# Performance work log

Measured on AMD Instinct MI355X. Metric: run time of the kernel, lower is better.

Reference implementation:

```python
import jax, jax.numpy as jnp
import numpy as np

N_RAYS = 65536
S_UNIFORM = 256          # 2 * n_samples coarse samples per ray
N_IMP = 128              # importance samples per ray
TRUNCATION = 2.0 / 512.0 * 4.0  # default in sdf2weights


def raw2weights_occupancy(raw):
    # raw2outputs_nerf_color with occupancy=True
    alpha = jax.nn.sigmoid(10.0 * raw)  # [N, S]
    trans = jnp.cumprod(
        jnp.concatenate([jnp.ones_like(alpha[:, :1]), 1.0 - alpha + 1e-10], axis=-1),
        axis=-1,
    )[:, :-1]
    return alpha, alpha * trans


def sample_pdf_det(bins, weights, n_samples):
    # bins: [N, M], weights: [N, M-1]; deterministic (det=True) inverse-CDF sampling
    w = weights + 1e-5
    pdf = w / jnp.sum(w, axis=-1, keepdims=True)
    cdf = jnp.cumsum(pdf, axis=-1)
    cdf = jnp.concatenate([jnp.zeros_like(cdf[..., :1]), cdf], axis=-1)  # [N, M]
    u = jnp.linspace(0.0, 1.0, n_samples, dtype=cdf.dtype)
    u = jnp.broadcast_to(u, cdf.shape[:-1] + (n_samples,))               # [N, n]
    inds = jax.vmap(lambda c, uu: jnp.searchsorted(c, uu, side='right'))(cdf, u)
    below = jnp.maximum(inds - 1, 0)
    above = jnp.minimum(inds, cdf.shape[-1] - 1)
    cdf_b = jnp.take_along_axis(cdf, below, axis=-1)
    cdf_a = jnp.take_along_axis(cdf, above, axis=-1)
    bins_b = jnp.take_along_axis(bins, below, axis=-1)
    bins_a = jnp.take_along_axis(bins, above, axis=-1)
    denom = cdf_a - cdf_b
    denom = jnp.where(denom < 1e-5, jnp.ones_like(denom), denom)
    t = (u - cdf_b) / denom
    return bins_b + t * (bins_a - bins_b)


def sdf2weights(sdf, z_vals, truncation=TRUNCATION, sc_factor=1.0):
    alpha = jax.nn.sigmoid(sdf / truncation) * jax.nn.sigmoid(-sdf / truncation)
    signs = sdf[:, 1:] * sdf[:, :-1]
    sign_mask = jnp.where(signs < 0.0, 1.0, 0.0)
    inds = jnp.argmax(sign_mask, axis=1)[:, None]              # first zero-crossing
    z_min = jnp.take_along_axis(z_vals, inds, axis=1)          # [N, 1]
    trunc_mask = jnp.where(z_vals < z_min + sc_factor * truncation, 1.0, 0.0)
    alpha = alpha * trunc_mask
    weights = alpha / (jnp.sum(alpha, axis=-1, keepdims=True) + 1e-8)
    return weights


def setup_inputs() -> dict:
    key = jax.random.key(0)
    k1, k2, k3, k4 = jax.random.split(key, 4)
    occ = jax.random.normal(k1, (N_RAYS, S_UNIFORM), dtype=jnp.float32)
    # monotonically increasing depths in [0.1, 4.1)
    z_vals_u = jnp.sort(
        jax.random.uniform(k2, (N_RAYS, S_UNIFORM), dtype=jnp.float32) * 4.0 + 0.1,
        axis=-1,
    )
    sdf = jax.random.normal(k3, (N_RAYS, N_IMP), dtype=jnp.float32) * 0.05
    rgbs = jax.random.uniform(k4, (N_RAYS, N_IMP, 3), dtype=jnp.float32)
    return {"occ": occ, "z_vals_u": z_vals_u, "sdf": sdf, "rgbs": rgbs}


def reference(occ, z_vals_u, sdf, rgbs):
    # 1) coarse occupancy compositing -> weights
    _, w_u = raw2weights_occupancy(occ)
    # 2) inverse-CDF importance sampling over midpoints (detached, as in gen_samples)
    z_mid = 0.5 * (z_vals_u[..., 1:] + z_vals_u[..., :-1])
    z_samples = jax.lax.stop_gradient(sample_pdf_det(z_mid, w_u[..., 1:-1], N_IMP))
    # 3) TSDF weights at importance samples
    weights = sdf2weights(sdf, z_samples)
    # 4) composite
    rgb_map = jnp.clip(jnp.sum(weights[..., None] * rgbs, axis=-2), 0.0, 1.0)  # [N,3]
    depth_map = jnp.sum(weights * z_samples, axis=-1)                          # [N]
    return jnp.concatenate([rgb_map, depth_map[:, None], weights], axis=-1)    # [N, 4+N_IMP]
```

## Files before the change

### kernel.cpp

```cpp
#include <hip/hip_runtime.h>

#define S_U 256
#define N_IMP 128
#define OUT_STRIDE (4 + N_IMP)
#define TRUNC 0.015625f
#define WPB 4

__device__ __forceinline__ float inv_cdf_sample(const float* __restrict__ cdf,
                                                const float* __restrict__ zm,
                                                float u) {
    int lo = 0, hi = 255;
#pragma unroll
    for (int it = 0; it < 8; ++it) {
        int mid = (lo + hi) >> 1;
        bool c = cdf[mid] <= u;
        lo = c ? mid + 1 : lo;
        hi = c ? hi : mid;
    }
    int below = max(lo - 1, 0);
    int above = min(lo, 254);
    float cb = cdf[below], ca = cdf[above];
    float zb = zm[below],  za = zm[above];
    float denom = ca - cb;
    denom = (denom < 1e-5f) ? 1.0f : denom;
    float t = (u - cb) / denom;
    return zb + t * (za - zb);
}

__global__ __launch_bounds__(256) void tsdf_render_kernel(
    const float* __restrict__ occ,
    const float* __restrict__ zvals,
    const float* __restrict__ sdf,
    const float* __restrict__ rgbs,
    float* __restrict__ out)
{
    const int lane = threadIdx.x & 63;
    const int wv   = threadIdx.x >> 6;
    const int ray  = blockIdx.x * WPB + wv;

    __shared__ __align__(16) float s_cdf [WPB][S_U];
    __shared__ __align__(16) float s_zmid[WPB][S_U];

    const float4 o4 = ((const float4*)(occ   + (size_t)ray * S_U))[lane];
    const float4 z4 = ((const float4*)(zvals + (size_t)ray * S_U))[lane];

    float a0 = 1.0f / (1.0f + __expf(-10.0f * o4.x));
    float a1 = 1.0f / (1.0f + __expf(-10.0f * o4.y));
    float a2 = 1.0f / (1.0f + __expf(-10.0f * o4.z));
    float a3 = 1.0f / (1.0f + __expf(-10.0f * o4.w));
    float t0 = 1.0f - a0 + 1e-10f;
    float t1 = 1.0f - a1 + 1e-10f;
    float t2 = 1.0f - a2 + 1e-10f;
    float t3 = 1.0f - a3 + 1e-10f;

    float pp0 = t0, pp1 = pp0 * t1, pp2 = pp1 * t2, pp3 = pp2 * t3;
    float ip = pp3;
#pragma unroll
    for (int d = 1; d < 64; d <<= 1) {
        float y = __shfl_up(ip, d);
        if (lane >= d) ip *= y;
    }
    float pbase = __shfl_up(ip, 1);
    if (lane == 0) pbase = 1.0f;

    float w0 = a0 * pbase;
    float w1 = a1 * pbase * pp0;
    float w2 = a2 * pbase * pp1;
    float w3 = a3 * pbase * pp2;

    float v0 = (lane > 0)  ? w0 + 1e-5f : 0.0f;
    float v1 = w1 + 1e-5f;
    float v2 = w2 + 1e-5f;
    float v3 = (lane < 63) ? w3 + 1e-5f : 0.0f;
    float s0 = v0, s1 = s0 + v1, s2 = s1 + v2, s3 = s2 + v3;
    float is = s3;
#pragma unroll
    for (int d = 1; d < 64; d <<= 1) {
        float y = __shfl_up(is, d);
        if (lane >= d) is += y;
    }
    float total = __shfl(is, 63);
    float sbase = __shfl_up(is, 1);
    if (lane == 0) sbase = 0.0f;
    float invt = 1.0f / total;

    float4 cdf4;
    cdf4.x = (sbase + s0) * invt;
    cdf4.y = (sbase + s1) * invt;
    cdf4.z = (sbase + s2) * invt;
    cdf4.w = (sbase + s3) * invt;
    *((float4*)&s_cdf[wv][lane * 4]) = cdf4;

    float znext = __shfl_down(z4.x, 1);
    float4 zm4;
    zm4.x = 0.5f * (z4.x + z4.y);
    zm4.y = 0.5f * (z4.y + z4.z);
    zm4.z = 0.5f * (z4.z + z4.w);
    zm4.w = 0.5f * (z4.w + znext);
    *((float4*)&s_zmid[wv][lane * 4]) = zm4;

    __builtin_amdgcn_wave_barrier();

    const float2 sd2 = ((const float2*)(sdf + (size_t)ray * N_IMP))[lane];
    const float2* rg = (const float2*)(rgbs + (size_t)ray * (N_IMP * 3)) + lane * 3;
    float2 p0 = rg[0];
    float2 p1 = rg[1];
    float2 p2 = rg[2];

    const float* cdfp = s_cdf[wv];
    const float* zmp  = s_zmid[wv];
    float u0 = (float)(2 * lane)     * (1.0f / 127.0f);
    float u1 = (float)(2 * lane + 1) * (1.0f / 127.0f);
    float zs0 = inv_cdf_sample(cdfp, zmp, u0);
    float zs1 = inv_cdf_sample(cdfp, zmp, u1);

    float sn = __shfl_down(sd2.x, 1);
    int c = 0x7fffffff;
    if (sd2.x * sd2.y < 0.0f)                     c = 2 * lane;
    else if (lane < 63 && sd2.y * sn < 0.0f)      c = 2 * lane + 1;
#pragma unroll
    for (int d = 32; d > 0; d >>= 1) c = min(c, __shfl_xor(c, d));
    int ci = (c == 0x7fffffff) ? 0 : c;
    float zca = __shfl(zs0, ci >> 1);
    float zcb = __shfl(zs1, ci >> 1);
    float z_min = (ci & 1) ? zcb : zca;

    float x0 = sd2.x * (1.0f / TRUNC);
    float x1 = sd2.y * (1.0f / TRUNC);
    float al0 = 1.0f / (2.0f + __expf(x0) + __expf(-x0));
    float al1 = 1.0f / (2.0f + __expf(x1) + __expf(-x1));
    float zlim = z_min + TRUNC;
    if (!(zs0 < zlim)) al0 = 0.0f;
    if (!(zs1 < zlim)) al1 = 0.0f;

    float asum = al0 + al1;
#pragma unroll
    for (int d = 32; d > 0; d >>= 1) asum += __shfl_xor(asum, d);
    float inv_s = 1.0f / (asum + 1e-8f);
    float g0 = al0 * inv_s;
    float g1 = al1 * inv_s;

    float rr = g0 * p0.x + g1 * p1.y;
    float gg = g0 * p0.y + g1 * p2.x;
    float bb = g0 * p1.x + g1 * p2.y;
    float dd = g0 * zs0  + g1 * zs1;
#pragma unroll
    for (int d = 32; d > 0; d >>= 1) {
        rr += __shfl_xor(rr, d);
        gg += __shfl_xor(gg, d);
        bb += __shfl_xor(bb, d);
        dd += __shfl_xor(dd, d);
    }

    float* ob = out + (size_t)ray * OUT_STRIDE;
    ((float2*)(ob + 4))[lane] = make_float2(g0, g1);
    if (lane == 0) {
        ob[0] = fminf(fmaxf(rr, 0.0f), 1.0f);
        ob[1] = fminf(fmaxf(gg, 0.0f), 1.0f);
        ob[2] = fminf(fmaxf(bb, 0.0f), 1.0f);
        ob[3] = dd;
    }
}

extern "C" void kernel_launch(void* const* d_in, const int* in_sizes, int n_in,
                              void* d_out, int out_size, void* d_ws, size_t ws_size,
                              hipStream_t stream) {
    const float* occ  = (const float*)d_in[0];
    const float* z    = (const float*)d_in[1];
    const float* sdf  = (const float*)d_in[2];
    const float* rgbs = (const float*)d_in[3];
    float* out = (float*)d_out;
    const int n_rays = in_sizes[0] / S_U;
    hipLaunchKernelGGL(tsdf_render_kernel, dim3(n_rays / WPB), dim3(256), 0, stream,
                       occ, z, sdf, rgbs, out);
}
```

Baseline: 266.2 us.

## Replace per-sample binary search with scatter-scan bin lookup and DPP wave scans

Swaps the 8-step binary search over the CDF for each importance sample for an inverted approach. Each CDF entry computes which uniform sample index it covers and scatters its bin index into shared memory, and a wave max-scan then gives each sample its bin. All shuffle-based scans and reductions become DPP row and broadcast operations, and all sdf and rgb global loads are moved to the kernel start. Divisions become hardware reciprocal approximations, which may change rounding slightly. The kernel is probably bound by memory bandwidth, so the lower ALU and LDS work may only partly show in the runtime.

```diff
diff --git a/kernel.cpp b/kernel.cpp
--- a/kernel.cpp
+++ b/kernel.cpp
@@ -1,30 +1,69 @@
 #include <hip/hip_runtime.h>
+#include <limits.h>
 
 #define S_U 256
 #define N_IMP 128
 #define OUT_STRIDE (4 + N_IMP)
 #define TRUNC 0.015625f
 #define WPB 4
-
-__device__ __forceinline__ float inv_cdf_sample(const float* __restrict__ cdf,
-                                                const float* __restrict__ zm,
-                                                float u) {
-    int lo = 0, hi = 255;
-#pragma unroll
-    for (int it = 0; it < 8; ++it) {
-        int mid = (lo + hi) >> 1;
-        bool c = cdf[mid] <= u;
-        lo = c ? mid + 1 : lo;
-        hi = c ? hi : mid;
-    }
-    int below = max(lo - 1, 0);
-    int above = min(lo, 254);
-    float cb = cdf[below], ca = cdf[above];
-    float zb = zm[below],  za = zm[above];
-    float denom = ca - cb;
-    denom = (denom < 1e-5f) ? 1.0f : denom;
-    float t = (u - cb) / denom;
-    return zb + t * (za - zb);
+#define INV127 (1.0f / 127.0f)
+
+template<int CTRL, int RM, int BM>
+__device__ __forceinline__ int dpp_i(int old_, int x) {
+    return __builtin_amdgcn_update_dpp(old_, x, CTRL, RM, BM, false);
+}
+template<int CTRL, int RM, int BM>
+__device__ __forceinline__ float dpp_f(float old_, float x) {
+    return __int_as_float(__builtin_amdgcn_update_dpp(
+        __float_as_int(old_), __float_as_int(x), CTRL, RM, BM, false));
+}
+__device__ __forceinline__ float readlane_f(float x, int l) {
+    return __int_as_float(__builtin_amdgcn_readlane(__float_as_int(x), l));
+}
+
+__device__ __forceinline__ float wscan_add(float x) {
+    x += dpp_f<0x111,0xf,0xf>(0.0f, x);
+    x += dpp_f<0x112,0xf,0xf>(0.0f, x);
+    x += dpp_f<0x114,0xf,0xf>(0.0f, x);
+    x += dpp_f<0x118,0xf,0xf>(0.0f, x);
+    x += dpp_f<0x142,0xa,0xf>(0.0f, x);
+    x += dpp_f<0x143,0xc,0xf>(0.0f, x);
+    return x;
+}
+__device__ __forceinline__ float wscan_mul(float x) {
+    x *= dpp_f<0x111,0xf,0xf>(1.0f, x);
+    x *= dpp_f<0x112,0xf,0xf>(1.0f, x);
+    x *= dpp_f<0x114,0xf,0xf>(1.0f, x);
+    x *= dpp_f<0x118,0xf,0xf>(1.0f, x);
+    x *= dpp_f<0x142,0xa,0xf>(1.0f, x);
+    x *= dpp_f<0x143,0xc,0xf>(1.0f, x);
+    return x;
+}
+__device__ __forceinline__ int wscan_max(int x) {
+    x = max(x, dpp_i<0x111,0xf,0xf>(0, x));
+    x = max(x, dpp_i<0x112,0xf,0xf>(0, x));
+    x = max(x, dpp_i<0x114,0xf,0xf>(0, x));
+    x = max(x, dpp_i<0x118,0xf,0xf>(0, x));
+    x = max(x, dpp_i<0x142,0xa,0xf>(0, x));
+    x = max(x, dpp_i<0x143,0xc,0xf>(0, x));
+    return x;
+}
+__device__ __forceinline__ int wred_min(int x) {
+    x = min(x, dpp_i<0x111,0xf,0xf>(INT_MAX, x));
+    x = min(x, dpp_i<0x112,0xf,0xf>(INT_MAX, x));
+    x = min(x, dpp_i<0x114,0xf,0xf>(INT_MAX, x));
+    x = min(x, dpp_i<0x118,0xf,0xf>(INT_MAX, x));
+    x = min(x, dpp_i<0x142,0xa,0xf>(INT_MAX, x));
+    x = min(x, dpp_i<0x143,0xc,0xf>(INT_MAX, x));
+    return x;
+}
+
+__device__ __forceinline__ int jm_of(float c) {
+    int jm = (int)ceilf(c * 127.0f);
+    jm = min(max(jm, 0), 128);
+    if (jm > 0 && (float)(jm - 1) * INV127 >= c) jm--;
+    else if (jm < 128 && (float)jm * INV127 < c) jm++;
+    return jm;
 }
 
 __global__ __launch_bounds__(256) void tsdf_render_kernel(
@@ -40,9 +79,15 @@
 
     __shared__ __align__(16) float s_cdf [WPB][S_U];
     __shared__ __align__(16) float s_zmid[WPB][S_U];
-
-    const float4 o4 = ((const float4*)(occ   + (size_t)ray * S_U))[lane];
-    const float4 z4 = ((const float4*)(zvals + (size_t)ray * S_U))[lane];
+    __shared__ __align__(16) int   s_bs  [WPB][N_IMP];
+
+    const float4 o4  = ((const float4*)(occ   + (size_t)ray * S_U))[lane];
+    const float4 z4  = ((const float4*)(zvals + (size_t)ray * S_U))[lane];
+    const float2 sd2 = ((const float2*)(sdf   + (size_t)ray * N_IMP))[lane];
+    const float2* rg = (const float2*)(rgbs + (size_t)ray * (N_IMP * 3)) + lane * 3;
+    const float2 p0 = rg[0];
+    const float2 p1 = rg[1];
+    const float2 p2 = rg[2];
 
     float a0 = 1.0f / (1.0f + __expf(-10.0f * o4.x));
     float a1 = 1.0f / (1.0f + __expf(-10.0f * o4.y));
@@ -54,14 +99,8 @@
     float t3 = 1.0f - a3 + 1e-10f;
 
     float pp0 = t0, pp1 = pp0 * t1, pp2 = pp1 * t2, pp3 = pp2 * t3;
-    float ip = pp3;
-#pragma unroll
-    for (int d = 1; d < 64; d <<= 1) {
-        float y = __shfl_up(ip, d);
-        if (lane >= d) ip *= y;
-    }
-    float pbase = __shfl_up(ip, 1);
-    if (lane == 0) pbase = 1.0f;
+    float P = wscan_mul(pp3);
+    float pbase = dpp_f<0x138,0xf,0xf>(1.0f, P);
 
     float w0 = a0 * pbase;
     float w1 = a1 * pbase * pp0;
@@ -73,15 +112,9 @@
     float v2 = w2 + 1e-5f;
     float v3 = (lane < 63) ? w3 + 1e-5f : 0.0f;
     float s0 = v0, s1 = s0 + v1, s2 = s1 + v2, s3 = s2 + v3;
-    float is = s3;
-#pragma unroll
-    for (int d = 1; d < 64; d <<= 1) {
-        float y = __shfl_up(is, d);
-        if (lane >= d) is += y;
-    }
-    float total = __shfl(is, 63);
-    float sbase = __shfl_up(is, 1);
-    if (lane == 0) sbase = 0.0f;
+    float S  = wscan_add(s3);
+    float sbase = dpp_f<0x138,0xf,0xf>(0.0f, S);
+    float total = readlane_f(S, 63);
     float invt = 1.0f / total;
 
     float4 cdf4;
@@ -91,7 +124,7 @@
     cdf4.w = (sbase + s3) * invt;
     *((float4*)&s_cdf[wv][lane * 4]) = cdf4;
 
-    float znext = __shfl_down(z4.x, 1);
+    float znext = dpp_f<0x130,0xf,0xf>(z4.x, z4.x);
     float4 zm4;
     zm4.x = 0.5f * (z4.x + z4.y);
     zm4.y = 0.5f * (z4.y + z4.z);
@@ -99,62 +132,81 @@
     zm4.w = 0.5f * (z4.w + znext);
     *((float4*)&s_zmid[wv][lane * 4]) = zm4;
 
+    *((int2*)&s_bs[wv][lane * 2]) = make_int2(0, 0);
+
     __builtin_amdgcn_wave_barrier();
 
-    const float2 sd2 = ((const float2*)(sdf + (size_t)ray * N_IMP))[lane];
-    const float2* rg = (const float2*)(rgbs + (size_t)ray * (N_IMP * 3)) + lane * 3;
-    float2 p0 = rg[0];
-    float2 p1 = rg[1];
-    float2 p2 = rg[2];
+    int jm0 = jm_of(cdf4.x);
+    int jm1 = jm_of(cdf4.y);
+    int jm2 = jm_of(cdf4.z);
+    int jm3 = jm_of(cdf4.w);
+    if (lane == 63) jm3 = 128;
+    int jmn = dpp_i<0x130,0xf,0xf>(128, jm0);
+
+    int ib = lane * 4;
+    if (jm0 < jm1) s_bs[wv][jm0] = ib;
+    if (jm1 < jm2) s_bs[wv][jm1] = ib + 1;
+    if (jm2 < jm3) s_bs[wv][jm2] = ib + 2;
+    if (jm3 < jmn) s_bs[wv][jm3] = ib + 3;
+
+    __builtin_amdgcn_wave_barrier();
+
+    int2 bse = *((const int2*)&s_bs[wv][lane * 2]);
+    int H  = wscan_max(max(bse.x, bse.y));
+    int Hp = dpp_i<0x138,0xf,0xf>(0, H);
+    int b0 = max(Hp, bse.x);
+    int b1 = H;
 
     const float* cdfp = s_cdf[wv];
     const float* zmp  = s_zmid[wv];
-    float u0 = (float)(2 * lane)     * (1.0f / 127.0f);
-    float u1 = (float)(2 * lane + 1) * (1.0f / 127.0f);
-    float zs0 = inv_cdf_sample(cdfp, zmp, u0);
-    float zs1 = inv_cdf_sample(cdfp, zmp, u1);
-
-    float sn = __shfl_down(sd2.x, 1);
-    int c = 0x7fffffff;
-    if (sd2.x * sd2.y < 0.0f)                     c = 2 * lane;
-    else if (lane < 63 && sd2.y * sn < 0.0f)      c = 2 * lane + 1;
-#pragma unroll
-    for (int d = 32; d > 0; d >>= 1) c = min(c, __shfl_xor(c, d));
-    int ci = (c == 0x7fffffff) ? 0 : c;
-    float zca = __shfl(zs0, ci >> 1);
-    float zcb = __shfl(zs1, ci >> 1);
-    float z_min = (ci & 1) ? zcb : zca;
+    float u0 = (float)(2 * lane)     * INV127;
+    float u1 = (float)(2 * lane + 1) * INV127;
+
+    float cb0 = cdfp[b0], ca0 = cdfp[b0 + 1];
+    float zb0 = zmp[b0],  za0 = zmp[b0 + 1];
+    float cb1 = cdfp[b1], ca1 = cdfp[b1 + 1];
+    float zb1 = zmp[b1],  za1 = zmp[b1 + 1];
+
+    float d0 = ca0 - cb0; d0 = (d0 < 1e-5f) ? 1.0f : d0;
+    float d1 = ca1 - cb1; d1 = (d1 < 1e-5f) ? 1.0f : d1;
+    float tt0 = (u0 - cb0) * __builtin_amdgcn_rcpf(d0);
+    float tt1 = (u1 - cb1) * __builtin_amdgcn_rcpf(d1);
+    float zs0 = zb0 + tt0 * (za0 - zb0);
+    float zs1 = zb1 + tt1 * (za1 - zb1);
+
+    float sn = dpp_f<0x130,0xf,0xf>(sd2.x, sd2.x);
+    int c = INT_MAX;
+    if (sd2.x * sd2.y < 0.0f)                  c = 2 * lane;
+    else if (lane < 63 && sd2.y * sn < 0.0f)   c = 2 * lane + 1;
+    c = wred_min(c);
+    int cis = __builtin_amdgcn_readlane(c, 63);
+    cis = (cis == INT_MAX) ? 0 : cis;
+    float zca = readlane_f(zs0, cis >> 1);
+    float zcb = readlane_f(zs1, cis >> 1);
+    float z_min = (cis & 1) ? zcb : zca;
 
     float x0 = sd2.x * (1.0f / TRUNC);
     float x1 = sd2.y * (1.0f / TRUNC);
-    float al0 = 1.0f / (2.0f + __expf(x0) + __expf(-x0));
-    float al1 = 1.0f / (2.0f + __expf(x1) + __expf(-x1));
+    float al0 = __builtin_amdgcn_rcpf(2.0f + __expf(x0) + __expf(-x0));
+    float al1 = __builtin_amdgcn_rcpf(2.0f + __expf(x1) + __expf(-x1));
     float zlim = z_min + TRUNC;
     if (!(zs0 < zlim)) al0 = 0.0f;
     if (!(zs1 < zlim)) al1 = 0.0f;
 
-    float asum = al0 + al1;
-#pragma unroll
-    for (int d = 32; d > 0; d >>= 1) asum += __shfl_xor(asum, d);
-    float inv_s = 1.0f / (asum + 1e-8f);
+    float At = wscan_add(al0 + al1);
+    float asum = readlane_f(At, 63);
+    float inv_s = __builtin_amdgcn_rcpf(asum + 1e-8f);
     float g0 = al0 * inv_s;
     float g1 = al1 * inv_s;
 
-    float rr = g0 * p0.x + g1 * p1.y;
-    float gg = g0 * p0.y + g1 * p2.x;
-    float bb = g0 * p1.x + g1 * p2.y;
-    float dd = g0 * zs0  + g1 * zs1;
-#pragma unroll
-    for (int d = 32; d > 0; d >>= 1) {
-        rr += __shfl_xor(rr, d);
-        gg += __shfl_xor(gg, d);
-        bb += __shfl_xor(bb, d);
-        dd += __shfl_xor(dd, d);
-    }
+    float rr = wscan_add(g0 * p0.x + g1 * p1.y);
+    float gg = wscan_add(g0 * p0.y + g1 * p2.x);
+    float bb = wscan_add(g0 * p1.x + g1 * p2.y);
+    float dd = wscan_add(g0 * zs0  + g1 * zs1);
 
     float* ob = out + (size_t)ray * OUT_STRIDE;
     ((float2*)(ob + 4))[lane] = make_float2(g0, g1);
-    if (lane == 0) {
+    if (lane == 63) {
         ob[0] = fminf(fmaxf(rr, 0.0f), 1.0f);
         ob[1] = fminf(fmaxf(gg, 0.0f), 1.0f);
         ob[2] = fminf(fmaxf(bb, 0.0f), 1.0f);
```

After: 267.2 us. No clear change (+0.4%).
